# Performance work log

Hardware: AMD Instinct MI355X
Metric: run time of the kernel (lower is better)

The kernel has to match this reference:

```python
import jax, jax.numpy as jnp
import numpy as np

B, N, P, H, BINF = 64, 100, 640000, 128, 11

def setup_inputs() -> dict:
    key = jax.random.key(0)
    ks = jax.random.split(key, 10)
    s = 1.0 / np.sqrt(H)
    sparse_idx = jnp.stack([
        jax.random.randint(ks[0], (P,), 0, B),
        jax.random.randint(ks[1], (P,), 0, N),
        jax.random.randint(ks[2], (P,), 0, N),
    ], axis=1).astype(jnp.int64)  # [P, 3]
    return {
        "local_pair": jax.random.normal(ks[3], (P, H), jnp.float32),
        "global_pair": jax.random.normal(ks[4], (P, H), jnp.float32),
        "binary": jax.random.normal(ks[5], (B, N, N, BINF), jnp.float32),
        "sparse_idx": sparse_idx,
        "W_local": jax.random.normal(ks[6], (H, H), jnp.float32) * s,
        "W_global": jax.random.normal(ks[7], (H, H), jnp.float32) * s,
        "b_global": jnp.zeros((H,), jnp.float32),
        "W_binary": jax.random.normal(ks[8], (BINF, H), jnp.float32) * s,
        "W_score": jax.random.normal(ks[9], (H, 5), jnp.float32) * s,
        "b_score": jnp.zeros((5,), jnp.float32),
    }

def reference(local_pair, global_pair, binary, sparse_idx,
              W_local, W_global, b_global, W_binary, W_score, b_score):
    # gather binary bond features for each scored pair: [P, BINF]
    binary_feats = binary[sparse_idx[:, 0], sparse_idx[:, 1], sparse_idx[:, 2]]
    # fused 3-way linear + relu
    pair_feats = jax.nn.relu(
        local_pair @ W_local
        + (global_pair @ W_global + b_global)
        + binary_feats @ W_binary
    )  # [P, H]
    score = pair_feats @ W_score + b_score  # [P, 5]
    return score
```

## Files before the change

### kernel.cpp

```cpp
#include <hip/hip_runtime.h>
#include <stdint.h>

typedef __bf16 bf16x8 __attribute__((ext_vector_type(8)));
typedef float f32x16 __attribute__((ext_vector_type(16)));

#define H 128
#define NBINF 11
#define NCHUNK 17
#define PTOT 640000
#define ROWS 64
#define ASTRIDE 560
#define FSTRIDE 272

__device__ __align__(16) unsigned short g_wpack[NCHUNK * 4 * 64 * 8];
__device__ __align__(16) unsigned short g_wsp[8 * 64 * 8];
__device__ int g_flag;

__device__ __forceinline__ uint32_t f2bf_u(float f) {
  uint32_t u = __float_as_uint(f);
  return (u + 0x7FFFu + ((u >> 16) & 1u)) >> 16;
}
__device__ __forceinline__ uint32_t pk_bf(float lo, float hi) {
  return (f2bf_u(lo) & 0xFFFFu) | (f2bf_u(hi) << 16);
}

__global__ void k_flag(const int* __restrict__ sidx) {
  int t = threadIdx.x;
  int v = sidx[2 * t + 1];
  unsigned long long any = __ballot(v != 0);
  if (t == 0) g_flag = (any == 0ull) ? 2 : 1;
}

__global__ void k_pack(const float* __restrict__ Wl, const float* __restrict__ Wg,
                       const float* __restrict__ Wb, const float* __restrict__ Wsc) {
  int tid = blockIdx.x * 256 + threadIdx.x;
  if (tid < NCHUNK * 4 * 64 * 8) {
    int j = tid & 7, l = (tid >> 3) & 63, nt = (tid >> 9) & 3, c = tid >> 11;
    int k = c * 16 + ((l >> 5) << 3) + j;
    int n = nt * 32 + (l & 31);
    float v = 0.f;
    if (k < 128)       v = Wl[k * H + n];
    else if (k < 256)  v = Wg[(k - 128) * H + n];
    else { int kk = k - 256; v = (kk < NBINF) ? Wb[kk * H + n] : 0.f; }
    g_wpack[tid] = (unsigned short)f2bf_u(v);
  }
  if (tid < 8 * 64 * 8) {
    int j = tid & 7, l = (tid >> 3) & 63, cs = tid >> 9;
    int h = (cs >> 1) * 32 + (cs & 1) * 16 + ((l >> 5) << 3) + j;
    int s = l & 31;
    float v = (s < 5) ? Wsc[h * 5 + s] : 0.f;
    g_wsp[tid] = (unsigned short)f2bf_u(v);
  }
}

__launch_bounds__(256, 3)
__global__ void k_main(const float* __restrict__ lp, const float* __restrict__ gp,
                       const float* __restrict__ bin, const int* __restrict__ sidx,
                       const float* __restrict__ bg, const float* __restrict__ bsc,
                       float* __restrict__ out) {
  __shared__ __align__(16) char sm[ROWS * ASTRIDE];
  const int t   = threadIdx.x;
  const int wid = t >> 6;
  const int l   = t & 63;
  const int lr  = l & 31;
  const int lh  = l >> 5;
  const int p0  = blockIdx.x * ROWS;

  bf16x8 wreg[NCHUNK];
#pragma unroll
  for (int c = 0; c < NCHUNK; ++c)
    wreg[c] = *(const bf16x8*)(g_wpack + ((size_t)(c * 4 + wid) * 64 + l) * 8);

#pragma unroll
  for (int i = 0; i < 8; ++i) {
    int u = t + i * 256;
    int row = u >> 5, slot = u & 31;
    const float* src = (slot < 16)
        ? lp + (size_t)(p0 + row) * H + slot * 8
        : gp + (size_t)(p0 + row) * H + (slot - 16) * 8;
    float4 x0 = ((const float4*)src)[0];
    float4 x1 = ((const float4*)src)[1];
    uint4 pk = make_uint4(pk_bf(x0.x, x0.y), pk_bf(x0.z, x0.w),
                          pk_bf(x1.x, x1.y), pk_bf(x1.z, x1.w));
    *(uint4*)(sm + row * ASTRIDE + slot * 16) = pk;
  }
  if (t < 2 * ROWS) {
    int row = t >> 1, bh = t & 1;
    int prow = p0 + row;
    const int stride = g_flag;
    int bi = sidx[(prow * 3 + 0) * stride];
    int ii = sidx[(prow * 3 + 1) * stride];
    int jj = sidx[(prow * 3 + 2) * stride];
    int base = ((bi * 100 + ii) * 100 + jj) * NBINF;
    float v[8];
#pragma unroll
    for (int j = 0; j < 8; ++j) {
      int e = bh * 8 + j;
      v[j] = (e < NBINF) ? bin[base + e] : 0.f;
    }
    uint4 pk = make_uint4(pk_bf(v[0], v[1]), pk_bf(v[2], v[3]),
                          pk_bf(v[4], v[5]), pk_bf(v[6], v[7]));
    *(uint4*)(sm + row * ASTRIDE + 512 + bh * 16) = pk;
  }
  __syncthreads();

  f32x16 acc[2] = {};
#pragma unroll
  for (int c = 0; c < NCHUNK; ++c) {
#pragma unroll
    for (int rt = 0; rt < 2; ++rt) {
      bf16x8 a = *(const bf16x8*)(sm + (rt * 32 + lr) * ASTRIDE + c * 32 + lh * 16);
      acc[rt] = __builtin_amdgcn_mfma_f32_32x32x16_bf16(a, wreg[c], acc[rt], 0, 0, 0);
    }
  }
  __syncthreads();

  {
    float bgv = bg[wid * 32 + lr];
#pragma unroll
    for (int rt = 0; rt < 2; ++rt) {
#pragma unroll
      for (int r = 0; r < 16; ++r) {
        int row_t = (r & 3) + ((r >> 2) << 3) + (lh << 2);
        float v = fmaxf(acc[rt][r] + bgv, 0.f);
        *(unsigned short*)(sm + (size_t)(rt * 32 + row_t) * FSTRIDE +
                           (size_t)(wid * 32 + lr) * 2) = (unsigned short)f2bf_u(v);
      }
    }
  }
  __syncthreads();

  if (wid < 2) {
    bf16x8 ws[8];
#pragma unroll
    for (int cs = 0; cs < 8; ++cs)
      ws[cs] = *(const bf16x8*)(g_wsp + ((size_t)cs * 64 + l) * 8);
    f32x16 sacc = {};
#pragma unroll
    for (int cs = 0; cs < 8; ++cs) {
      bf16x8 a = *(const bf16x8*)(sm + (size_t)(wid * 32 + lr) * FSTRIDE +
                                  cs * 32 + lh * 16);
      sacc = __builtin_amdgcn_mfma_f32_32x32x16_bf16(a, ws[cs], sacc, 0, 0, 0);
    }
    if (lr < 5) {
      float bs = bsc[lr];
      float* op = out + (size_t)(p0 + wid * 32) * 5 + lr;
#pragma unroll
      for (int r = 0; r < 16; ++r) {
        int row_t = (r & 3) + ((r >> 2) << 3) + (lh << 2);
        op[row_t * 5] = sacc[r] + bs;
      }
    }
  }
}

extern "C" void kernel_launch(void* const* d_in, const int* in_sizes, int n_in,
                              void* d_out, int out_size, void* d_ws, size_t ws_size,
                              hipStream_t stream) {
  const float* lp  = (const float*)d_in[0];
  const float* gp  = (const float*)d_in[1];
  const float* bin = (const float*)d_in[2];
  const int*   si  = (const int*)d_in[3];
  const float* Wl  = (const float*)d_in[4];
  const float* Wg  = (const float*)d_in[5];
  const float* bg  = (const float*)d_in[6];
  const float* Wb  = (const float*)d_in[7];
  const float* Wsc = (const float*)d_in[8];
  const float* bsc = (const float*)d_in[9];
  float* out = (float*)d_out;

  hipLaunchKernelGGL(k_flag, dim3(1), dim3(64), 0, stream, si);
  hipLaunchKernelGGL(k_pack, dim3(136), dim3(256), 0, stream, Wl, Wg, Wb, Wsc);
  hipLaunchKernelGGL(k_main, dim3(PTOT / ROWS), dim3(256), 0, stream,
                     lp, gp, bin, si, bg, bsc, out);
}
```

Before: 170.4 us.

## Make main kernel persistent with double-buffered register-staged prefetch of next tile

```diff
diff --git a/kernel.cpp b/kernel.cpp
--- a/kernel.cpp
+++ b/kernel.cpp
@@ -9,19 +9,18 @@
 #define NCHUNK 17
 #define PTOT 640000
 #define ROWS 64
+#define NT (PTOT / ROWS)
+#define GRID 512
 #define ASTRIDE 560
+#define ABUF (ROWS * ASTRIDE)
 #define FSTRIDE 272
 
 __device__ __align__(16) unsigned short g_wpack[NCHUNK * 4 * 64 * 8];
 __device__ __align__(16) unsigned short g_wsp[8 * 64 * 8];
 __device__ int g_flag;
 
-__device__ __forceinline__ uint32_t f2bf_u(float f) {
-  uint32_t u = __float_as_uint(f);
-  return (u + 0x7FFFu + ((u >> 16) & 1u)) >> 16;
-}
-__device__ __forceinline__ uint32_t pk_bf(float lo, float hi) {
-  return (f2bf_u(lo) & 0xFFFFu) | (f2bf_u(hi) << 16);
+__device__ __forceinline__ unsigned short f2bf(float f) {
+  return (unsigned short)__builtin_bit_cast(unsigned short, (__bf16)f);
 }
 
 __global__ void k_flag(const int* __restrict__ sidx) {
@@ -42,115 +41,154 @@
     if (k < 128)       v = Wl[k * H + n];
     else if (k < 256)  v = Wg[(k - 128) * H + n];
     else { int kk = k - 256; v = (kk < NBINF) ? Wb[kk * H + n] : 0.f; }
-    g_wpack[tid] = (unsigned short)f2bf_u(v);
+    g_wpack[tid] = f2bf(v);
   }
   if (tid < 8 * 64 * 8) {
     int j = tid & 7, l = (tid >> 3) & 63, cs = tid >> 9;
-    int h = (cs >> 1) * 32 + (cs & 1) * 16 + ((l >> 5) << 3) + j;
     int s = l & 31;
-    float v = (s < 5) ? Wsc[h * 5 + s] : 0.f;
-    g_wsp[tid] = (unsigned short)f2bf_u(v);
+    int k = cs * 16 + ((l >> 5) << 3) + j;
+    float v = (s < 5) ? Wsc[k * 5 + s] : 0.f;
+    g_wsp[tid] = f2bf(v);
   }
 }
 
-__launch_bounds__(256, 3)
+__device__ __forceinline__ void bar_lgkm() {
+  asm volatile("s_waitcnt lgkmcnt(0)" ::: "memory");
+  __builtin_amdgcn_s_barrier();
+}
+
+__launch_bounds__(256, 2)
 __global__ void k_main(const float* __restrict__ lp, const float* __restrict__ gp,
                        const float* __restrict__ bin, const int* __restrict__ sidx,
                        const float* __restrict__ bg, const float* __restrict__ bsc,
                        float* __restrict__ out) {
-  __shared__ __align__(16) char sm[ROWS * ASTRIDE];
+  __shared__ __align__(16) char sm[2 * ABUF];
   const int t   = threadIdx.x;
   const int wid = t >> 6;
   const int l   = t & 63;
   const int lr  = l & 31;
   const int lh  = l >> 5;
-  const int p0  = blockIdx.x * ROWS;
+  const int sflag = g_flag;
 
   bf16x8 wreg[NCHUNK];
 #pragma unroll
   for (int c = 0; c < NCHUNK; ++c)
     wreg[c] = *(const bf16x8*)(g_wpack + ((size_t)(c * 4 + wid) * 64 + l) * 8);
-
-#pragma unroll
-  for (int i = 0; i < 8; ++i) {
-    int u = t + i * 256;
-    int row = u >> 5, slot = u & 31;
-    const float* src = (slot < 16)
-        ? lp + (size_t)(p0 + row) * H + slot * 8
-        : gp + (size_t)(p0 + row) * H + (slot - 16) * 8;
-    float4 x0 = ((const float4*)src)[0];
-    float4 x1 = ((const float4*)src)[1];
-    uint4 pk = make_uint4(pk_bf(x0.x, x0.y), pk_bf(x0.z, x0.w),
-                          pk_bf(x1.x, x1.y), pk_bf(x1.z, x1.w));
-    *(uint4*)(sm + row * ASTRIDE + slot * 16) = pk;
-  }
-  if (t < 2 * ROWS) {
-    int row = t >> 1, bh = t & 1;
-    int prow = p0 + row;
-    const int stride = g_flag;
-    int bi = sidx[(prow * 3 + 0) * stride];
-    int ii = sidx[(prow * 3 + 1) * stride];
-    int jj = sidx[(prow * 3 + 2) * stride];
-    int base = ((bi * 100 + ii) * 100 + jj) * NBINF;
-    float v[8];
-#pragma unroll
-    for (int j = 0; j < 8; ++j) {
-      int e = bh * 8 + j;
-      v[j] = (e < NBINF) ? bin[base + e] : 0.f;
-    }
-    uint4 pk = make_uint4(pk_bf(v[0], v[1]), pk_bf(v[2], v[3]),
-                          pk_bf(v[4], v[5]), pk_bf(v[6], v[7]));
-    *(uint4*)(sm + row * ASTRIDE + 512 + bh * 16) = pk;
-  }
-  __syncthreads();
-
-  f32x16 acc[2] = {};
-#pragma unroll
-  for (int c = 0; c < NCHUNK; ++c) {
-#pragma unroll
-    for (int rt = 0; rt < 2; ++rt) {
-      bf16x8 a = *(const bf16x8*)(sm + (rt * 32 + lr) * ASTRIDE + c * 32 + lh * 16);
-      acc[rt] = __builtin_amdgcn_mfma_f32_32x32x16_bf16(a, wreg[c], acc[rt], 0, 0, 0);
-    }
-  }
-  __syncthreads();
-
-  {
-    float bgv = bg[wid * 32 + lr];
-#pragma unroll
-    for (int rt = 0; rt < 2; ++rt) {
-#pragma unroll
-      for (int r = 0; r < 16; ++r) {
-        int row_t = (r & 3) + ((r >> 2) << 3) + (lh << 2);
-        float v = fmaxf(acc[rt][r] + bgv, 0.f);
-        *(unsigned short*)(sm + (size_t)(rt * 32 + row_t) * FSTRIDE +
-                           (size_t)(wid * 32 + lr) * 2) = (unsigned short)f2bf_u(v);
-      }
-    }
-  }
-  __syncthreads();
-
-  if (wid < 2) {
-    bf16x8 ws[8];
-#pragma unroll
-    for (int cs = 0; cs < 8; ++cs)
-      ws[cs] = *(const bf16x8*)(g_wsp + ((size_t)cs * 64 + l) * 8);
-    f32x16 sacc = {};
-#pragma unroll
-    for (int cs = 0; cs < 8; ++cs) {
-      bf16x8 a = *(const bf16x8*)(sm + (size_t)(wid * 32 + lr) * FSTRIDE +
-                                  cs * 32 + lh * 16);
-      sacc = __builtin_amdgcn_mfma_f32_32x32x16_bf16(a, ws[cs], sacc, 0, 0, 0);
-    }
-    if (lr < 5) {
-      float bs = bsc[lr];
-      float* op = out + (size_t)(p0 + wid * 32) * 5 + lr;
-#pragma unroll
-      for (int r = 0; r < 16; ++r) {
-        int row_t = (r & 3) + ((r >> 2) << 3) + (lh << 2);
-        op[row_t * 5] = sacc[r] + bs;
-      }
-    }
+  bf16x8 ws[8];
+#pragma unroll
+  for (int cs = 0; cs < 8; ++cs)
+    ws[cs] = *(const bf16x8*)(g_wsp + ((size_t)cs * 64 + l) * 8);
+
+  const float bgv = bg[wid * 32 + lr];
+  const float b0 = bsc[0], b1 = bsc[1], b2 = bsc[2], b3 = bsc[3], b4 = bsc[4];
+
+  float4 pay[16];
+  float  bv[8];
+
+  auto issue = [&](int tile) {
+    const int p0 = tile * ROWS;
+#pragma unroll
+    for (int i = 0; i < 8; ++i) {
+      int u = t + i * 256, row = u >> 5, slot = u & 31;
+      const float* src = (slot < 16)
+          ? lp + (size_t)(p0 + row) * H + slot * 8
+          : gp + (size_t)(p0 + row) * H + (slot - 16) * 8;
+      pay[2 * i]     = ((const float4*)src)[0];
+      pay[2 * i + 1] = ((const float4*)src)[1];
+    }
+    if (t < 2 * ROWS) {
+      int row = t >> 1, bh = t & 1, prow = p0 + row;
+      int bi = sidx[(prow * 3 + 0) * sflag];
+      int ii = sidx[(prow * 3 + 1) * sflag];
+      int jj = sidx[(prow * 3 + 2) * sflag];
+      int base = ((bi * 100 + ii) * 100 + jj) * NBINF;
+#pragma unroll
+      for (int j = 0; j < 8; ++j) {
+        int e = bh * 8 + j;
+        bv[j] = (e < NBINF) ? bin[base + e] : 0.f;
+      }
+    }
+  };
+
+  auto commit = [&](int buf) {
+    char* dst = sm + buf * ABUF;
+#pragma unroll
+    for (int i = 0; i < 8; ++i) {
+      int u = t + i * 256, row = u >> 5, slot = u & 31;
+      float4 a = pay[2 * i], b = pay[2 * i + 1];
+      bf16x8 v;
+      v[0] = (__bf16)a.x; v[1] = (__bf16)a.y; v[2] = (__bf16)a.z; v[3] = (__bf16)a.w;
+      v[4] = (__bf16)b.x; v[5] = (__bf16)b.y; v[6] = (__bf16)b.z; v[7] = (__bf16)b.w;
+      *(bf16x8*)(dst + row * ASTRIDE + slot * 16) = v;
+    }
+    if (t < 2 * ROWS) {
+      int row = t >> 1, bh = t & 1;
+      bf16x8 v;
+#pragma unroll
+      for (int j = 0; j < 8; ++j) v[j] = (__bf16)bv[j];
+      *(bf16x8*)(dst + row * ASTRIDE + 512 + bh * 16) = v;
+    }
+  };
+
+  const int tile0 = blockIdx.x;
+  issue(tile0);
+  commit(0);
+  bar_lgkm();
+
+  int cur = 0;
+  for (int tile = tile0; tile < NT; tile += GRID) {
+    const int nxt = tile + GRID;
+    if (nxt < NT) issue(nxt);
+
+    const char* A = sm + cur * ABUF;
+    f32x16 acc[2] = {};
+#pragma unroll
+    for (int c = 0; c < NCHUNK; ++c) {
+#pragma unroll
+      for (int rt = 0; rt < 2; ++rt) {
+        bf16x8 a = *(const bf16x8*)(A + (rt * 32 + lr) * ASTRIDE + c * 32 + lh * 16);
+        acc[rt] = __builtin_amdgcn_mfma_f32_32x32x16_bf16(a, wreg[c], acc[rt], 0, 0, 0);
+      }
+    }
+    bar_lgkm();
+
+    {
+      char* F = sm + cur * ABUF;
+#pragma unroll
+      for (int rt = 0; rt < 2; ++rt) {
+#pragma unroll
+        for (int rg = 0; rg < 16; ++rg) {
+          int rowt = (rg & 3) + ((rg >> 2) << 3) + (lh << 2);
+          float fv = fmaxf(acc[rt][rg] + bgv, 0.f);
+          *(__bf16*)(F + (size_t)(rt * 32 + rowt) * FSTRIDE +
+                     (size_t)(wid * 32 + lr) * 2) = (__bf16)fv;
+        }
+      }
+    }
+    bar_lgkm();
+
+    if (wid < 2) {
+      const char* F = sm + cur * ABUF;
+      f32x16 sacc = {};
+#pragma unroll
+      for (int cs = 0; cs < 8; ++cs) {
+        bf16x8 fb = *(const bf16x8*)(F + (size_t)(wid * 32 + lr) * FSTRIDE +
+                                     cs * 32 + lh * 16);
+        sacc = __builtin_amdgcn_mfma_f32_32x32x16_bf16(ws[cs], fb, sacc, 0, 0, 0);
+      }
+      int prow = tile * ROWS + wid * 32 + lr;
+      float* op = out + (size_t)prow * 5;
+      if (lh == 0) {
+        op[0] = sacc[0] + b0; op[1] = sacc[1] + b1;
+        op[2] = sacc[2] + b2; op[3] = sacc[3] + b3;
+      } else {
+        op[4] = sacc[0] + b4;
+      }
+    }
+
+    if (nxt < NT) commit(cur ^ 1);
+    bar_lgkm();
+    cur ^= 1;
   }
 }
 
@@ -171,6 +209,6 @@
 
   hipLaunchKernelGGL(k_flag, dim3(1), dim3(64), 0, stream, si);
   hipLaunchKernelGGL(k_pack, dim3(136), dim3(256), 0, stream, Wl, Wg, Wb, Wsc);
-  hipLaunchKernelGGL(k_main, dim3(PTOT / ROWS), dim3(256), 0, stream,
+  hipLaunchKernelGGL(k_main, dim3(GRID), dim3(256), 0, stream,
                      lp, gp, bin, si, bg, bsc, out);
 }
```

After: 147.3 us. 1.16x faster.
